# Kernel optimization log

Hardware: AMD Instinct MI355X
Metric: run time of the kernel (lower is better)

Reference implementation:

```python
import jax, jax.numpy as jnp
import numpy as np

HIDDEN = 768
HEADS = 12
HEAD_DIM = HIDDEN // HEADS
INTER = 1152
WINDOW = 128
EPS = 1e-5
ROPE_WAVELENGTH = 10000.0


def setup_inputs() -> dict:
    key = jax.random.key(0)
    ks = jax.random.split(key, 8)
    B, S = 2, 2048
    x = jax.random.normal(ks[0], (B, S, HIDDEN), dtype=jnp.float32)
    padding_mask = jnp.ones((B, S), dtype=jnp.int32)
    sc = 0.02
    wqkv = jax.random.normal(ks[1], (HIDDEN, 3 * HIDDEN), dtype=jnp.float32) * sc
    wo_attn = jax.random.normal(ks[2], (HIDDEN, HIDDEN), dtype=jnp.float32) * sc
    wi0 = jax.random.normal(ks[3], (HIDDEN, INTER), dtype=jnp.float32) * sc
    wi1 = jax.random.normal(ks[4], (HIDDEN, INTER), dtype=jnp.float32) * sc
    wo_mlp = jax.random.normal(ks[5], (INTER, HIDDEN), dtype=jnp.float32) * sc
    g_attn = jnp.ones((HIDDEN,), dtype=jnp.float32)
    g_mlp = jnp.ones((HIDDEN,), dtype=jnp.float32)
    return dict(x=x, padding_mask=padding_mask, wqkv=wqkv, wo_attn=wo_attn,
                wi0=wi0, wi1=wi1, wo_mlp=wo_mlp, g_attn=g_attn, g_mlp=g_mlp)


def _rmsnorm(x, gamma):
    # Keras LayerNormalization(rms_scaling=True): x * rsqrt(mean(x^2)+eps) * gamma
    inv = jax.lax.rsqrt(jnp.mean(jnp.square(x), axis=-1, keepdims=True) + EPS)
    return x * inv * gamma


def _rope(t):
    # t: [B, S, H, D]; standard rotate-half RoPE over the head dim
    S, D = t.shape[1], t.shape[3]
    inv_freq = 1.0 / (ROPE_WAVELENGTH ** (jnp.arange(0, D, 2, dtype=jnp.float32) / D))
    freqs = jnp.arange(S, dtype=jnp.float32)[:, None] * inv_freq[None, :]  # [S, D/2]
    emb = jnp.concatenate([freqs, freqs], axis=-1)  # [S, D]
    cos = jnp.cos(emb)[None, :, None, :]
    sin = jnp.sin(emb)[None, :, None, :]
    h1, h2 = jnp.split(t, 2, axis=-1)
    rot = jnp.concatenate([-h2, h1], axis=-1)
    return t * cos + rot * sin


def reference(x, padding_mask, wqkv, wo_attn, wi0, wi1, wo_mlp, g_attn, g_mlp):
    B, S, _ = x.shape
    # --- attention sub-block ---
    res = x
    h = _rmsnorm(x, g_attn)
    qkv = (h @ wqkv).reshape(B, S, 3, HEADS, HEAD_DIM)
    q, k, v = qkv[:, :, 0], qkv[:, :, 1], qkv[:, :, 2]  # [B, S, H, D]
    q = _rope(q)
    k = _rope(k)
    scores = jnp.einsum('bqhd,bkhd->bhqk', q, k) / jnp.sqrt(
        jnp.asarray(HEAD_DIM, x.dtype))
    pos = jnp.arange(S)
    window = (jnp.abs(pos[:, None] - pos[None, :]) <= WINDOW // 2).astype(jnp.float32)
    mask = window[None, None, :, :] * padding_mask.astype(jnp.float32)[:, None, None, :]
    scores = scores + (1.0 - mask) * -1e9
    attn = jax.nn.softmax(scores, axis=-1)
    out = jnp.einsum('bhqk,bkhd->bqhd', attn, v).reshape(B, S, HIDDEN)
    x = res + out @ wo_attn
    # --- GeGLU MLP sub-block ---
    res = x
    h = _rmsnorm(x, g_mlp)
    h = jax.nn.gelu(h @ wi0, approximate=True) * (h @ wi1)
    return res + h @ wo_mlp
```

## Files before the change

### kernel.cpp

```cpp
#include <hip/hip_runtime.h>
#include <hip/hip_bf16.h>

#define HID 768
#define NHEADS 12
#define HD 64
#define INTER 1152
#define SEQ 2048
#define NB 2
#define ROWS (NB * SEQ)
#define QTA 64
#define KTA 192

typedef __attribute__((ext_vector_type(8))) short bf16x8;
typedef __attribute__((ext_vector_type(4))) float f32x4;

__device__ __forceinline__ float bf2f(unsigned short u) {
    union { unsigned int i; float f; } c; c.i = ((unsigned int)u) << 16; return c.f;
}
__device__ __forceinline__ unsigned short f2bf(float f) {
    union { float f; unsigned int i; } c; c.f = f;
    unsigned int b = c.i;
    b += 0x7FFFu + ((b >> 16) & 1u);
    return (unsigned short)(b >> 16);
}
__device__ __forceinline__ void gload16(const void* g, void* l) {
    __builtin_amdgcn_global_load_lds((const __attribute__((address_space(1))) unsigned int*)g,
                                     (__attribute__((address_space(3))) unsigned int*)l,
                                     16, 0, 0);
}

__global__ __launch_bounds__(256) void rmsnorm_kernel(const float* __restrict__ x,
                                                      const float* __restrict__ g,
                                                      unsigned short* __restrict__ out) {
    int row = blockIdx.x;
    const float* xr = x + (size_t)row * HID;
    unsigned short* orow = out + (size_t)row * HID;
    int tid = threadIdx.x;
    float v0 = xr[tid], v1 = xr[tid + 256], v2 = xr[tid + 512];
    float s = v0 * v0 + v1 * v1 + v2 * v2;
    #pragma unroll
    for (int m = 32; m >= 1; m >>= 1) s += __shfl_xor(s, m, 64);
    __shared__ float red[4];
    if ((tid & 63) == 0) red[tid >> 6] = s;
    __syncthreads();
    float tot = red[0] + red[1] + red[2] + red[3];
    float inv = rsqrtf(tot * (1.0f / HID) + 1e-5f);
    orow[tid]       = f2bf(v0 * inv * g[tid]);
    orow[tid + 256] = f2bf(v1 * inv * g[tid + 256]);
    orow[tid + 512] = f2bf(v2 * inv * g[tid + 512]);
}

__device__ __forceinline__ void wt_tile(const float* __restrict__ W,
                                        unsigned short* __restrict__ Wt,
                                        int K, int N, int bx, int by,
                                        float (*t)[33]) {
    int tx = threadIdx.x & 31, ty = threadIdx.x >> 5;
    #pragma unroll
    for (int i = 0; i < 4; ++i)
        t[ty + i * 8][tx] = W[(size_t)(by * 32 + ty + i * 8) * N + bx * 32 + tx];
    __syncthreads();
    #pragma unroll
    for (int i = 0; i < 4; ++i)
        Wt[(size_t)(bx * 32 + ty + i * 8) * K + by * 32 + tx] = f2bf(t[tx][ty + i * 8]);
}

__global__ __launch_bounds__(256) void prep_kernel(const float* __restrict__ wqkv,
                                                   const float* __restrict__ woa,
                                                   const float* __restrict__ wi0,
                                                   const float* __restrict__ wi1,
                                                   const float* __restrict__ wom,
                                                   unsigned short* __restrict__ wqkvT,
                                                   unsigned short* __restrict__ woaT,
                                                   unsigned short* __restrict__ wi0T,
                                                   unsigned short* __restrict__ wi1T,
                                                   unsigned short* __restrict__ womT,
                                                   float2* __restrict__ rtab) {
    __shared__ float t[32][33];
    int id = blockIdx.x;
    if (id < 1728)       wt_tile(wqkv, wqkvT, 768, 2304, id % 72, id / 72, t);
    else if (id < 2304)  { id -= 1728; wt_tile(woa, woaT, 768, 768, id % 24, id / 24, t); }
    else if (id < 3168)  { id -= 2304; wt_tile(wi0, wi0T, 768, 1152, id % 36, id / 36, t); }
    else if (id < 4032)  { id -= 3168; wt_tile(wi1, wi1T, 768, 1152, id % 36, id / 36, t); }
    else if (id < 4896)  { id -= 4032; wt_tile(wom, womT, 1152, 768, id % 24, id / 24, t); }
    else {
        int idx = (id - 4896) * 256 + threadIdx.x;
        int s = idx >> 5, fi = idx & 31;
        float ang = (float)s * exp2f(-(float)fi * 0.41524101186f);
        float sn, cs;
        sincosf(ang, &sn, &cs);
        rtab[idx] = make_float2(cs, sn);
    }
}

__global__ __launch_bounds__(256) void mfma_gemm64(const unsigned short* __restrict__ A,
                                                   const unsigned short* __restrict__ Bt,
                                                   const float* __restrict__ resid,
                                                   float* __restrict__ C,
                                                   int N, int K, int nbx) {
    __shared__ unsigned short As[64 * 64];
    __shared__ unsigned short Bs[64 * 64];
    int nwg = gridDim.x;
    int bid = blockIdx.x;
    int id2 = (bid & 7) * (nwg >> 3) + (bid >> 3);
    int row0 = (id2 / nbx) * 64, col0 = (id2 % nbx) * 64;
    int tid = threadIdx.x;
    int wave = tid >> 6, lane = tid & 63;
    int wr = wave >> 1, wc = wave & 1;
    int fr = lane & 15, fq = lane >> 4;

    f32x4 acc[2][2];
    #pragma unroll
    for (int m = 0; m < 2; ++m)
        #pragma unroll
        for (int n = 0; n < 2; ++n)
            acc[m][n] = (f32x4){0.f, 0.f, 0.f, 0.f};

    const size_t strideA = (size_t)K * 2;
    const char* Ab = (const char*)A;
    const char* Bb = (const char*)Bt;

    for (int k0 = 0; k0 < K; k0 += 64) {
        #pragma unroll
        for (int r = 0; r < 2; ++r) {
            int L = r * 4096 + tid * 16;
            int row = L >> 7;
            int ss = ((L >> 4) & 7) ^ (row & 7);
            gload16(Ab + (size_t)(row0 + row) * strideA + (size_t)k0 * 2 + ss * 16,
                    (char*)As + L);
            gload16(Bb + (size_t)(col0 + row) * strideA + (size_t)k0 * 2 + ss * 16,
                    (char*)Bs + L);
        }
        __syncthreads();
        bf16x8 af[2][2], bff[2][2];
        #pragma unroll
        for (int m = 0; m < 2; ++m)
            #pragma unroll
            for (int kk = 0; kk < 2; ++kk) {
                int rowa = wr * 32 + m * 16 + fr;
                af[m][kk] = *(const bf16x8*)&As[rowa * 64 + ((kk * 4 + fq) ^ (rowa & 7)) * 8];
                int rowb = wc * 32 + m * 16 + fr;
                bff[m][kk] = *(const bf16x8*)&Bs[rowb * 64 + ((kk * 4 + fq) ^ (rowb & 7)) * 8];
            }
        #pragma unroll
        for (int m = 0; m < 2; ++m)
            #pragma unroll
            for (int n = 0; n < 2; ++n) {
                acc[m][n] = __builtin_amdgcn_mfma_f32_16x16x32_bf16(af[m][0], bff[n][0], acc[m][n], 0, 0, 0);
                acc[m][n] = __builtin_amdgcn_mfma_f32_16x16x32_bf16(af[m][1], bff[n][1], acc[m][n], 0, 0, 0);
            }
        __syncthreads();
    }

    #pragma unroll
    for (int m = 0; m < 2; ++m) {
        #pragma unroll
        for (int j = 0; j < 4; ++j) {
            size_t r = (size_t)(row0 + wr * 32 + m * 16 + fq * 4 + j);
            #pragma unroll
            for (int n = 0; n < 2; ++n) {
                size_t idx = r * N + (col0 + wc * 32 + n * 16 + fr);
                float v = acc[m][n][j];
                if (resid) v += resid[idx];
                C[idx] = v;
            }
        }
    }
}

__global__ __launch_bounds__(256) void gemm_qkv128(const unsigned short* __restrict__ A,
                                                   const unsigned short* __restrict__ Bt,
                                                   const float2* __restrict__ rtab,
                                                   unsigned short* __restrict__ Qb,
                                                   unsigned short* __restrict__ Kb,
                                                   unsigned short* __restrict__ Vt) {
    __shared__ unsigned short As[128 * 64];
    __shared__ unsigned short Bs[64 * 64];
    int bid = blockIdx.x;
    int id2 = (bid & 7) * 144 + (bid >> 3);
    int col0 = (id2 % 36) * 64, row0 = (id2 / 36) * 128;
    int tid = threadIdx.x;
    int wave = tid >> 6, lane = tid & 63;
    int fr = lane & 15, fq = lane >> 4;
    int type = col0 / 768;
    int h = (col0 % 768) >> 6;
    int b = row0 >> 11;
    int s0 = row0 & 2047;
    int bh = b * NHEADS + h;

    f32x4 acc[2][4];
    #pragma unroll
    for (int m = 0; m < 2; ++m)
        #pragma unroll
        for (int n = 0; n < 4; ++n)
            acc[m][n] = (f32x4){0.f, 0.f, 0.f, 0.f};

    const size_t strideA = (size_t)768 * 2;
    const char* Ab = (const char*)A;
    const char* Bb = (const char*)Bt;

    for (int k0 = 0; k0 < 768; k0 += 64) {
        #pragma unroll
        for (int r = 0; r < 4; ++r) {
            int L = r * 4096 + tid * 16;
            int row = L >> 7;
            int ss = ((L >> 4) & 7) ^ (row & 7);
            gload16(Ab + (size_t)(row0 + row) * strideA + (size_t)k0 * 2 + ss * 16,
                    (char*)As + L);
        }
        #pragma unroll
        for (int r = 0; r < 2; ++r) {
            int L = r * 4096 + tid * 16;
            int row = L >> 7;
            int ss = ((L >> 4) & 7) ^ (row & 7);
            gload16(Bb + (size_t)(col0 + row) * strideA + (size_t)k0 * 2 + ss * 16,
                    (char*)Bs + L);
        }
        __syncthreads();
        #pragma unroll
        for (int kk = 0; kk < 2; ++kk) {
            bf16x8 af[2], bf[4];
            #pragma unroll
            for (int m = 0; m < 2; ++m) {
                int rowa = wave * 32 + m * 16 + fr;
                af[m] = *(const bf16x8*)&As[rowa * 64 + ((kk * 4 + fq) ^ (rowa & 7)) * 8];
            }
            #pragma unroll
            for (int n = 0; n < 4; ++n) {
                int rowb = n * 16 + fr;
                bf[n] = *(const bf16x8*)&Bs[rowb * 64 + ((kk * 4 + fq) ^ (rowb & 7)) * 8];
            }
            #pragma unroll
            for (int m = 0; m < 2; ++m)
                #pragma unroll
                for (int n = 0; n < 4; ++n)
                    acc[m][n] = __builtin_amdgcn_mfma_f32_16x16x32_bf16(af[m], bf[n], acc[m][n], 0, 0, 0);
        }
        __syncthreads();
    }

    if (type < 2) {
        unsigned short* P = (type == 0 ? Qb : Kb) + ((size_t)bh * SEQ) * 64;
        #pragma unroll
        for (int m = 0; m < 2; ++m)
            #pragma unroll
            for (int n = 0; n < 4; ++n) {
                int d = n * 16 + fr;
                int fi = d & 31;
                #pragma unroll
                for (int j = 0; j < 4; ++j) {
                    int s = s0 + wave * 32 + m * 16 + fq * 4 + j;
                    float2 cs = rtab[s * 32 + fi];
                    float val = acc[m][n][j], par = acc[m][n ^ 2][j];
                    float o = (d < 32) ? val * cs.x - par * cs.y
                                       : val * cs.x + par * cs.y;
                    P[(size_t)s * 64 + d] = f2bf(o);
                }
            }
    } else {
        unsigned short* vt = As;
        #pragma unroll
        for (int m = 0; m < 2; ++m)
            #pragma unroll
            for (int n = 0; n < 4; ++n) {
                int d = n * 16 + fr;
                #pragma unroll
                for (int j = 0; j < 4; ++j)
                    vt[d * 136 + wave * 32 + m * 16 + fq * 4 + j] = f2bf(acc[m][n][j]);
            }
        __syncthreads();
        int d = tid >> 2, sg = tid & 3;
        unsigned short* vrow = Vt + ((size_t)bh * 64 + d) * SEQ + s0 + sg * 32;
        #pragma unroll
        for (int i = 0; i < 4; ++i)
            *(bf16x8*)(vrow + i * 8) = *(const bf16x8*)&vt[d * 136 + sg * 32 + i * 8];
    }
}

__global__ __launch_bounds__(256) void gemm_ffn128(const unsigned short* __restrict__ A,
                                                   const unsigned short* __restrict__ B0t,
                                                   const unsigned short* __restrict__ B1t,
                                                   unsigned short* __restrict__ O) {
    __shared__ unsigned short As[128 * 64];
    __shared__ unsigned short Bs0[64 * 64];
    __shared__ unsigned short Bs1[64 * 64];
    int bid = blockIdx.x;
    int id2 = (bid & 7) * 72 + (bid >> 3);
    int col0 = (id2 % 18) * 64, row0 = (id2 / 18) * 128;
    int tid = threadIdx.x;
    int wave = tid >> 6, lane = tid & 63;
    int fr = lane & 15, fq = lane >> 4;

    f32x4 acc0[2][4], acc1[2][4];
    #pragma unroll
    for (int m = 0; m < 2; ++m)
        #pragma unroll
        for (int n = 0; n < 4; ++n) {
            acc0[m][n] = (f32x4){0.f, 0.f, 0.f, 0.f};
            acc1[m][n] = (f32x4){0.f, 0.f, 0.f, 0.f};
        }

    const size_t strideA = (size_t)768 * 2;
    const char* Ab  = (const char*)A;
    const char* B0b = (const char*)B0t;
    const char* B1b = (const char*)B1t;

    for (int k0 = 0; k0 < 768; k0 += 64) {
        #pragma unroll
        for (int r = 0; r < 4; ++r) {
            int L = r * 4096 + tid * 16;
            int row = L >> 7;
            int ss = ((L >> 4) & 7) ^ (row & 7);
            gload16(Ab + (size_t)(row0 + row) * strideA + (size_t)k0 * 2 + ss * 16,
                    (char*)As + L);
        }
        #pragma unroll
        for (int r = 0; r < 2; ++r) {
            int L = r * 4096 + tid * 16;
            int row = L >> 7;
            int ss = ((L >> 4) & 7) ^ (row & 7);
            size_t goff = (size_t)(col0 + row) * strideA + (size_t)k0 * 2 + ss * 16;
            gload16(B0b + goff, (char*)Bs0 + L);
            gload16(B1b + goff, (char*)Bs1 + L);
        }
        __syncthreads();
        #pragma unroll
        for (int kk = 0; kk < 2; ++kk) {
            bf16x8 af[2], b0[4], b1[4];
            #pragma unroll
            for (int m = 0; m < 2; ++m) {
                int rowa = wave * 32 + m * 16 + fr;
                af[m] = *(const bf16x8*)&As[rowa * 64 + ((kk * 4 + fq) ^ (rowa & 7)) * 8];
            }
            #pragma unroll
            for (int n = 0; n < 4; ++n) {
                int rowb = n * 16 + fr;
                int sl = ((kk * 4 + fq) ^ (rowb & 7)) * 8;
                b0[n] = *(const bf16x8*)&Bs0[rowb * 64 + sl];
                b1[n] = *(const bf16x8*)&Bs1[rowb * 64 + sl];
            }
            #pragma unroll
            for (int m = 0; m < 2; ++m)
                #pragma unroll
                for (int n = 0; n < 4; ++n) {
                    acc0[m][n] = __builtin_amdgcn_mfma_f32_16x16x32_bf16(af[m], b0[n], acc0[m][n], 0, 0, 0);
                    acc1[m][n] = __builtin_amdgcn_mfma_f32_16x16x32_bf16(af[m], b1[n], acc1[m][n], 0, 0, 0);
                }
        }
        __syncthreads();
    }

    #pragma unroll
    for (int m = 0; m < 2; ++m)
        #pragma unroll
        for (int n = 0; n < 4; ++n)
            #pragma unroll
            for (int j = 0; j < 4; ++j) {
                int r = row0 + wave * 32 + m * 16 + fq * 4 + j;
                float xa = acc0[m][n][j];
                float tn = tanhf(0.7978845608028654f * (xa + 0.044715f * xa * xa * xa));
                float gv = 0.5f * xa * (1.f + tn) * acc1[m][n][j];
                O[(size_t)r * INTER + col0 + n * 16 + fr] = f2bf(gv);
            }
}

__global__ __launch_bounds__(256) void attn_mfma(const unsigned short* __restrict__ Qb,
                                                 const unsigned short* __restrict__ Kb,
                                                 const unsigned short* __restrict__ Vt,
                                                 const int* __restrict__ pmask,
                                                 unsigned short* __restrict__ ao) {
    __shared__ unsigned short Ks[KTA * 64];
    __shared__ unsigned short Vs[64 * KTA];
    __shared__ unsigned short Ps[4][16 * KTA];
    __shared__ float pmsk[KTA];

    int bid = blockIdx.x;
    int qt = bid & 31;
    int h  = (bid >> 5) % NHEADS;
    int b  = bid / (32 * NHEADS);
    int bh = b * NHEADS + h;
    int q0 = qt * QTA;
    int kstart = q0 - 64;
    int tid = threadIdx.x;
    int wave = tid >> 6, lane = tid & 63;
    int fr = lane & 15, fq = lane >> 4;

    const unsigned short* Kg = Kb + ((size_t)bh * SEQ) * 64;
    const unsigned short* Vg = Vt + ((size_t)bh * 64) * SEQ;

    if (tid < KTA) {
        int k = kstart + tid;
        pmsk[tid] = (k >= 0 && k < SEQ) ? (1.0f - (float)pmask[b * SEQ + k]) * -1e9f
                                        : -1e9f;
    }

    bool interior = (qt != 0) && (qt != 31);
    if (interior) {
        #pragma unroll
        for (int r = 0; r < 6; ++r) {
            int c = r * 256 + tid;
            int row = c >> 3, slot = c & 7;
            int ss = slot ^ (row & 7);
            gload16(Kg + (size_t)(kstart + row) * 64 + ss * 8, (char*)Ks + c * 16);
        }
        #pragma unroll
        for (int r = 0; r < 6; ++r) {
            int c = r * 256 + tid;
            int d = c / 24, slot = c - d * 24;
            int ss = (slot & ~7) | ((slot & 7) ^ (d & 7));
            gload16(Vg + (size_t)d * SEQ + kstart + ss * 8, (char*)Vs + c * 16);
        }
    } else {
        #pragma unroll
        for (int r = 0; r < 6; ++r) {
            int c = r * 256 + tid;
            int row = c >> 3, slot = c & 7;
            int ss = slot ^ (row & 7);
            int sk = kstart + row;
            bf16x8 val = {0, 0, 0, 0, 0, 0, 0, 0};
            if (sk >= 0 && sk < SEQ)
                val = *(const bf16x8*)(Kg + (size_t)sk * 64 + ss * 8);
            *(bf16x8*)((char*)Ks + c * 16) = val;
        }
        #pragma unroll
        for (int r = 0; r < 6; ++r) {
            int c = r * 256 + tid;
            int d = c / 24, slot = c - d * 24;
            int ss = (slot & ~7) | ((slot & 7) ^ (d & 7));
            int start = kstart + ss * 8;
            bf16x8 val = {0, 0, 0, 0, 0, 0, 0, 0};
            if (start >= 0 && start + 8 <= SEQ)
                val = *(const bf16x8*)(Vg + (size_t)d * SEQ + start);
            *(bf16x8*)((char*)Vs + c * 16) = val;
        }
    }
    __syncthreads();

    const unsigned short* Qg = Qb + ((size_t)bh * SEQ + q0 + wave * 16 + fr) * 64 + fq * 8;
    bf16x8 qf0 = *(const bf16x8*)(Qg);
    bf16x8 qf1 = *(const bf16x8*)(Qg + 32);

    f32x4 sc[12];
    #pragma unroll
    for (int n = 0; n < 12; ++n) sc[n] = (f32x4){0.f, 0.f, 0.f, 0.f};
    #pragma unroll
    for (int n = 0; n < 12; ++n) {
        int row = n * 16 + fr;
        int base = row * 64;
        bf16x8 k0 = *(const bf16x8*)&Ks[base + ((fq)     ^ (row & 7)) * 8];
        bf16x8 k1 = *(const bf16x8*)&Ks[base + ((4 + fq) ^ (row & 7)) * 8];
        sc[n] = __builtin_amdgcn_mfma_f32_16x16x32_bf16(qf0, k0, sc[n], 0, 0, 0);
        sc[n] = __builtin_amdgcn_mfma_f32_16x16x32_bf16(qf1, k1, sc[n], 0, 0, 0);
    }

    int qrow_base = q0 + wave * 16 + fq * 4;
    float mj[4] = {-1e30f, -1e30f, -1e30f, -1e30f}, sj[4];
    #pragma unroll
    for (int n = 0; n < 12; ++n) {
        int k = kstart + n * 16 + fr;
        float pm = pmsk[n * 16 + fr];
        #pragma unroll
        for (int j = 0; j < 4; ++j) {
            int diff = qrow_base + j - k;
            float s = sc[n][j] * 0.125f + pm;
            if (diff > 64 || diff < -64) s = -1e30f;
            sc[n][j] = s;
            mj[j] = fmaxf(mj[j], s);
        }
    }
    #pragma unroll
    for (int j = 0; j < 4; ++j) {
        #pragma unroll
        for (int mk = 1; mk < 16; mk <<= 1)
            mj[j] = fmaxf(mj[j], __shfl_xor(mj[j], mk, 16));
        sj[j] = 0.f;
    }
    #pragma unroll
    for (int n = 0; n < 12; ++n)
        #pragma unroll
        for (int j = 0; j < 4; ++j) {
            float e = expf(sc[n][j] - mj[j]);
            sc[n][j] = e;
            sj[j] += e;
        }
    #pragma unroll
    for (int j = 0; j < 4; ++j)
        #pragma unroll
        for (int mk = 1; mk < 16; mk <<= 1)
            sj[j] += __shfl_xor(sj[j], mk, 16);

    unsigned short* Pw = Ps[wave];
    #pragma unroll
    for (int n = 0; n < 12; ++n) {
        int slot = n * 2 + (fr >> 3);
        #pragma unroll
        for (int j = 0; j < 4; ++j) {
            int row = fq * 4 + j;
            int ss = (slot & ~7) | ((slot & 7) ^ (row & 7));
            Pw[row * KTA + ss * 8 + (fr & 7)] = f2bf(sc[n][j]);
        }
    }

    f32x4 oacc[4];
    #pragma unroll
    for (int n = 0; n < 4; ++n) oacc[n] = (f32x4){0.f, 0.f, 0.f, 0.f};
    #pragma unroll
    for (int kt = 0; kt < 6; ++kt) {
        int slot = kt * 4 + fq;
        int ssp = (slot & ~7) | ((slot & 7) ^ (fr & 7));
        bf16x8 pa = *(const bf16x8*)&Pw[fr * KTA + ssp * 8];
        #pragma unroll
        for (int n = 0; n < 4; ++n) {
            int d = n * 16 + fr;
            int ssv = (slot & ~7) | ((slot & 7) ^ (d & 7));
            bf16x8 vf = *(const bf16x8*)&Vs[d * KTA + ssv * 8];
            oacc[n] = __builtin_amdgcn_mfma_f32_16x16x32_bf16(pa, vf, oacc[n], 0, 0, 0);
        }
    }

    unsigned short* aob = ao + ((size_t)(b * SEQ + qrow_base)) * HID + h * 64;
    float rs[4];
    #pragma unroll
    for (int j = 0; j < 4; ++j) rs[j] = 1.0f / sj[j];
    #pragma unroll
    for (int n = 0; n < 4; ++n)
        #pragma unroll
        for (int j = 0; j < 4; ++j)
            aob[(size_t)j * HID + n * 16 + fr] = f2bf(oacc[n][j] * rs[j]);
}

extern "C" void kernel_launch(void* const* d_in, const int* in_sizes, int n_in,
                              void* d_out, int out_size, void* d_ws, size_t ws_size,
                              hipStream_t stream) {
    const float* x       = (const float*)d_in[0];
    const int*   pmask   = (const int*)d_in[1];
    const float* wqkv    = (const float*)d_in[2];
    const float* wo_attn = (const float*)d_in[3];
    const float* wi0     = (const float*)d_in[4];
    const float* wi1     = (const float*)d_in[5];
    const float* wo_mlp  = (const float*)d_in[6];
    const float* g_attn  = (const float*)d_in[7];
    const float* g_mlp   = (const float*)d_in[8];
    float* out = (float*)d_out;

    char* w = (char*)d_ws;
    unsigned short* hbf   = (unsigned short*)(w);
    unsigned short* aobf  = (unsigned short*)(w + 6291456);
    unsigned short* Qb    = (unsigned short*)(w + 12582912);
    unsigned short* Kb    = (unsigned short*)(w + 18874368);
    unsigned short* Vt    = (unsigned short*)(w + 25165824);
    unsigned short* mgate = (unsigned short*)(w + 31457280);
    float2*         rtab  = (float2*)(w + 40894464);
    unsigned short* wqkvT = (unsigned short*)(w + 41418752);
    unsigned short* woaT  = (unsigned short*)(w + 44957696);
    unsigned short* wi0T  = (unsigned short*)(w + 46137344);
    unsigned short* wi1T  = (unsigned short*)(w + 47906816);
    unsigned short* womT  = (unsigned short*)(w + 49676288);

    prep_kernel<<<5152, 256, 0, stream>>>(wqkv, wo_attn, wi0, wi1, wo_mlp,
                                          wqkvT, woaT, wi0T, wi1T, womT, rtab);
    rmsnorm_kernel<<<ROWS, 256, 0, stream>>>(x, g_attn, hbf);
    gemm_qkv128<<<1152, 256, 0, stream>>>(hbf, wqkvT, rtab, Qb, Kb, Vt);
    attn_mfma<<<NB * NHEADS * (SEQ / QTA), 256, 0, stream>>>(Qb, Kb, Vt, pmask, aobf);
    mfma_gemm64<<<768, 256, 0, stream>>>(aobf, woaT, x, out, 768, 768, 12);
    rmsnorm_kernel<<<ROWS, 256, 0, stream>>>(out, g_mlp, hbf);
    gemm_ffn128<<<576, 256, 0, stream>>>(hbf, wi0T, wi1T, mgate);
    mfma_gemm64<<<768, 256, 0, stream>>>(mgate, womT, out, out, 768, 1152, 12);
}
```

Baseline: 128.3 us.

## Merge weight prep with first RMSNorm, widen GEMM K-tiles, hoist Q loads

Folds the first RMSNorm into the weight-transpose/RoPE-table prep kernel so one launch does both. mfma_gemm64 and gemm_qkv128 now stage 128-wide K tiles in LDS with a 16-way XOR swizzle, which halves the barrier and loop count. The price is double the LDS per block, which can reduce occupancy. The attention kernel now issues the Q fragment loads before K/V staging so their latency overlaps.

```diff
diff --git a/kernel.cpp b/kernel.cpp
--- a/kernel.cpp
+++ b/kernel.cpp
@@ -29,6 +29,70 @@
                                      16, 0, 0);
 }
 
+__device__ __forceinline__ void wt_tile(const float* __restrict__ W,
+                                        unsigned short* __restrict__ Wt,
+                                        int K, int N, int bx, int by,
+                                        float (*t)[33]) {
+    int tx = threadIdx.x & 31, ty = threadIdx.x >> 5;
+    #pragma unroll
+    for (int i = 0; i < 4; ++i)
+        t[ty + i * 8][tx] = W[(size_t)(by * 32 + ty + i * 8) * N + bx * 32 + tx];
+    __syncthreads();
+    #pragma unroll
+    for (int i = 0; i < 4; ++i)
+        Wt[(size_t)(bx * 32 + ty + i * 8) * K + by * 32 + tx] = f2bf(t[tx][ty + i * 8]);
+}
+
+__global__ __launch_bounds__(256) void prep_rms_kernel(const float* __restrict__ x,
+                                                       const float* __restrict__ g,
+                                                       unsigned short* __restrict__ hbf,
+                                                       const float* __restrict__ wqkv,
+                                                       const float* __restrict__ woa,
+                                                       const float* __restrict__ wi0,
+                                                       const float* __restrict__ wi1,
+                                                       const float* __restrict__ wom,
+                                                       unsigned short* __restrict__ wqkvT,
+                                                       unsigned short* __restrict__ woaT,
+                                                       unsigned short* __restrict__ wi0T,
+                                                       unsigned short* __restrict__ wi1T,
+                                                       unsigned short* __restrict__ womT,
+                                                       float2* __restrict__ rtab) {
+    __shared__ float t[32][33];
+    __shared__ float red[4];
+    int id = blockIdx.x;
+    int tid = threadIdx.x;
+    if (id < 4096) {
+        const float* xr = x + (size_t)id * HID;
+        unsigned short* orow = hbf + (size_t)id * HID;
+        float v0 = xr[tid], v1 = xr[tid + 256], v2 = xr[tid + 512];
+        float s = v0 * v0 + v1 * v1 + v2 * v2;
+        #pragma unroll
+        for (int m = 32; m >= 1; m >>= 1) s += __shfl_xor(s, m, 64);
+        if ((tid & 63) == 0) red[tid >> 6] = s;
+        __syncthreads();
+        float tot = red[0] + red[1] + red[2] + red[3];
+        float inv = rsqrtf(tot * (1.0f / HID) + 1e-5f);
+        orow[tid]       = f2bf(v0 * inv * g[tid]);
+        orow[tid + 256] = f2bf(v1 * inv * g[tid + 256]);
+        orow[tid + 512] = f2bf(v2 * inv * g[tid + 512]);
+        return;
+    }
+    id -= 4096;
+    if (id < 1728)       wt_tile(wqkv, wqkvT, 768, 2304, id % 72, id / 72, t);
+    else if (id < 2304)  { id -= 1728; wt_tile(woa, woaT, 768, 768, id % 24, id / 24, t); }
+    else if (id < 3168)  { id -= 2304; wt_tile(wi0, wi0T, 768, 1152, id % 36, id / 36, t); }
+    else if (id < 4032)  { id -= 3168; wt_tile(wi1, wi1T, 768, 1152, id % 36, id / 36, t); }
+    else if (id < 4896)  { id -= 4032; wt_tile(wom, womT, 1152, 768, id % 24, id / 24, t); }
+    else {
+        int idx = (id - 4896) * 256 + tid;
+        int s = idx >> 5, fi = idx & 31;
+        float ang = (float)s * exp2f(-(float)fi * 0.41524101186f);
+        float sn, cs;
+        sincosf(ang, &sn, &cs);
+        rtab[idx] = make_float2(cs, sn);
+    }
+}
+
 __global__ __launch_bounds__(256) void rmsnorm_kernel(const float* __restrict__ x,
                                                       const float* __restrict__ g,
                                                       unsigned short* __restrict__ out) {
@@ -50,55 +114,13 @@
     orow[tid + 512] = f2bf(v2 * inv * g[tid + 512]);
 }
 
-__device__ __forceinline__ void wt_tile(const float* __restrict__ W,
-                                        unsigned short* __restrict__ Wt,
-                                        int K, int N, int bx, int by,
-                                        float (*t)[33]) {
-    int tx = threadIdx.x & 31, ty = threadIdx.x >> 5;
-    #pragma unroll
-    for (int i = 0; i < 4; ++i)
-        t[ty + i * 8][tx] = W[(size_t)(by * 32 + ty + i * 8) * N + bx * 32 + tx];
-    __syncthreads();
-    #pragma unroll
-    for (int i = 0; i < 4; ++i)
-        Wt[(size_t)(bx * 32 + ty + i * 8) * K + by * 32 + tx] = f2bf(t[tx][ty + i * 8]);
-}
-
-__global__ __launch_bounds__(256) void prep_kernel(const float* __restrict__ wqkv,
-                                                   const float* __restrict__ woa,
-                                                   const float* __restrict__ wi0,
-                                                   const float* __restrict__ wi1,
-                                                   const float* __restrict__ wom,
-                                                   unsigned short* __restrict__ wqkvT,
-                                                   unsigned short* __restrict__ woaT,
-                                                   unsigned short* __restrict__ wi0T,
-                                                   unsigned short* __restrict__ wi1T,
-                                                   unsigned short* __restrict__ womT,
-                                                   float2* __restrict__ rtab) {
-    __shared__ float t[32][33];
-    int id = blockIdx.x;
-    if (id < 1728)       wt_tile(wqkv, wqkvT, 768, 2304, id % 72, id / 72, t);
-    else if (id < 2304)  { id -= 1728; wt_tile(woa, woaT, 768, 768, id % 24, id / 24, t); }
-    else if (id < 3168)  { id -= 2304; wt_tile(wi0, wi0T, 768, 1152, id % 36, id / 36, t); }
-    else if (id < 4032)  { id -= 3168; wt_tile(wi1, wi1T, 768, 1152, id % 36, id / 36, t); }
-    else if (id < 4896)  { id -= 4032; wt_tile(wom, womT, 1152, 768, id % 24, id / 24, t); }
-    else {
-        int idx = (id - 4896) * 256 + threadIdx.x;
-        int s = idx >> 5, fi = idx & 31;
-        float ang = (float)s * exp2f(-(float)fi * 0.41524101186f);
-        float sn, cs;
-        sincosf(ang, &sn, &cs);
-        rtab[idx] = make_float2(cs, sn);
-    }
-}
-
 __global__ __launch_bounds__(256) void mfma_gemm64(const unsigned short* __restrict__ A,
                                                    const unsigned short* __restrict__ Bt,
                                                    const float* __restrict__ resid,
                                                    float* __restrict__ C,
                                                    int N, int K, int nbx) {
-    __shared__ unsigned short As[64 * 64];
-    __shared__ unsigned short Bs[64 * 64];
+    __shared__ unsigned short As[64 * 128];
+    __shared__ unsigned short Bs[64 * 128];
     int nwg = gridDim.x;
     int bid = blockIdx.x;
     int id2 = (bid & 7) * (nwg >> 3) + (bid >> 3);
@@ -108,46 +130,47 @@
     int wr = wave >> 1, wc = wave & 1;
     int fr = lane & 15, fq = lane >> 4;
 
-    f32x4 acc[2][2];
-    #pragma unroll
-    for (int m = 0; m < 2; ++m)
-        #pragma unroll
-        for (int n = 0; n < 2; ++n)
-            acc[m][n] = (f32x4){0.f, 0.f, 0.f, 0.f};
-
     const size_t strideA = (size_t)K * 2;
     const char* Ab = (const char*)A;
     const char* Bb = (const char*)Bt;
 
-    for (int k0 = 0; k0 < K; k0 += 64) {
-        #pragma unroll
-        for (int r = 0; r < 2; ++r) {
+    f32x4 acc[2][2];
+    #pragma unroll
+    for (int m = 0; m < 2; ++m)
+        #pragma unroll
+        for (int n = 0; n < 2; ++n)
+            acc[m][n] = (f32x4){0.f, 0.f, 0.f, 0.f};
+
+    int nt = K >> 7;
+    for (int t = 0; t < nt; ++t) {
+        int k0 = t << 7;
+        #pragma unroll
+        for (int r = 0; r < 4; ++r) {
             int L = r * 4096 + tid * 16;
-            int row = L >> 7;
-            int ss = ((L >> 4) & 7) ^ (row & 7);
+            int row = L >> 8;
+            int ss = ((L >> 4) & 15) ^ (row & 15);
             gload16(Ab + (size_t)(row0 + row) * strideA + (size_t)k0 * 2 + ss * 16,
                     (char*)As + L);
             gload16(Bb + (size_t)(col0 + row) * strideA + (size_t)k0 * 2 + ss * 16,
                     (char*)Bs + L);
         }
         __syncthreads();
-        bf16x8 af[2][2], bff[2][2];
-        #pragma unroll
-        for (int m = 0; m < 2; ++m)
-            #pragma unroll
-            for (int kk = 0; kk < 2; ++kk) {
+        #pragma unroll
+        for (int kk = 0; kk < 4; ++kk) {
+            bf16x8 af[2], bff[2];
+            #pragma unroll
+            for (int m = 0; m < 2; ++m) {
                 int rowa = wr * 32 + m * 16 + fr;
-                af[m][kk] = *(const bf16x8*)&As[rowa * 64 + ((kk * 4 + fq) ^ (rowa & 7)) * 8];
+                af[m] = *(const bf16x8*)&As[rowa * 128 + (((kk * 4 + fq)) ^ (rowa & 15)) * 8];
                 int rowb = wc * 32 + m * 16 + fr;
-                bff[m][kk] = *(const bf16x8*)&Bs[rowb * 64 + ((kk * 4 + fq) ^ (rowb & 7)) * 8];
-            }
-        #pragma unroll
-        for (int m = 0; m < 2; ++m)
-            #pragma unroll
-            for (int n = 0; n < 2; ++n) {
-                acc[m][n] = __builtin_amdgcn_mfma_f32_16x16x32_bf16(af[m][0], bff[n][0], acc[m][n], 0, 0, 0);
-                acc[m][n] = __builtin_amdgcn_mfma_f32_16x16x32_bf16(af[m][1], bff[n][1], acc[m][n], 0, 0, 0);
-            }
+                bff[m] = *(const bf16x8*)&Bs[rowb * 128 + (((kk * 4 + fq)) ^ (rowb & 15)) * 8];
+            }
+            #pragma unroll
+            for (int m = 0; m < 2; ++m)
+                #pragma unroll
+                for (int n = 0; n < 2; ++n)
+                    acc[m][n] = __builtin_amdgcn_mfma_f32_16x16x32_bf16(af[m], bff[n], acc[m][n], 0, 0, 0);
+        }
         __syncthreads();
     }
 
@@ -173,8 +196,8 @@
                                                    unsigned short* __restrict__ Qb,
                                                    unsigned short* __restrict__ Kb,
                                                    unsigned short* __restrict__ Vt) {
-    __shared__ unsigned short As[128 * 64];
-    __shared__ unsigned short Bs[64 * 64];
+    __shared__ unsigned short As[128 * 128];
+    __shared__ unsigned short Bs[64 * 128];
     int bid = blockIdx.x;
     int id2 = (bid & 7) * 144 + (bid >> 3);
     int col0 = (id2 % 36) * 64, row0 = (id2 / 36) * 128;
@@ -187,47 +210,48 @@
     int s0 = row0 & 2047;
     int bh = b * NHEADS + h;
 
-    f32x4 acc[2][4];
-    #pragma unroll
-    for (int m = 0; m < 2; ++m)
-        #pragma unroll
-        for (int n = 0; n < 4; ++n)
-            acc[m][n] = (f32x4){0.f, 0.f, 0.f, 0.f};
-
     const size_t strideA = (size_t)768 * 2;
     const char* Ab = (const char*)A;
     const char* Bb = (const char*)Bt;
 
-    for (int k0 = 0; k0 < 768; k0 += 64) {
+    f32x4 acc[2][4];
+    #pragma unroll
+    for (int m = 0; m < 2; ++m)
+        #pragma unroll
+        for (int n = 0; n < 4; ++n)
+            acc[m][n] = (f32x4){0.f, 0.f, 0.f, 0.f};
+
+    for (int t = 0; t < 6; ++t) {
+        int k0 = t << 7;
+        #pragma unroll
+        for (int r = 0; r < 8; ++r) {
+            int L = r * 4096 + tid * 16;
+            int row = L >> 8;
+            int ss = ((L >> 4) & 15) ^ (row & 15);
+            gload16(Ab + (size_t)(row0 + row) * strideA + (size_t)k0 * 2 + ss * 16,
+                    (char*)As + L);
+        }
         #pragma unroll
         for (int r = 0; r < 4; ++r) {
             int L = r * 4096 + tid * 16;
-            int row = L >> 7;
-            int ss = ((L >> 4) & 7) ^ (row & 7);
-            gload16(Ab + (size_t)(row0 + row) * strideA + (size_t)k0 * 2 + ss * 16,
-                    (char*)As + L);
-        }
-        #pragma unroll
-        for (int r = 0; r < 2; ++r) {
-            int L = r * 4096 + tid * 16;
-            int row = L >> 7;
-            int ss = ((L >> 4) & 7) ^ (row & 7);
+            int row = L >> 8;
+            int ss = ((L >> 4) & 15) ^ (row & 15);
             gload16(Bb + (size_t)(col0 + row) * strideA + (size_t)k0 * 2 + ss * 16,
                     (char*)Bs + L);
         }
         __syncthreads();
         #pragma unroll
-        for (int kk = 0; kk < 2; ++kk) {
+        for (int kk = 0; kk < 4; ++kk) {
             bf16x8 af[2], bf[4];
             #pragma unroll
             for (int m = 0; m < 2; ++m) {
                 int rowa = wave * 32 + m * 16 + fr;
-                af[m] = *(const bf16x8*)&As[rowa * 64 + ((kk * 4 + fq) ^ (rowa & 7)) * 8];
+                af[m] = *(const bf16x8*)&As[rowa * 128 + ((kk * 4 + fq) ^ (rowa & 15)) * 8];
             }
             #pragma unroll
             for (int n = 0; n < 4; ++n) {
                 int rowb = n * 16 + fr;
-                bf[n] = *(const bf16x8*)&Bs[rowb * 64 + ((kk * 4 + fq) ^ (rowb & 7)) * 8];
+                bf[n] = *(const bf16x8*)&Bs[rowb * 128 + ((kk * 4 + fq) ^ (rowb & 15)) * 8];
             }
             #pragma unroll
             for (int m = 0; m < 2; ++m)
@@ -387,6 +411,9 @@
     const unsigned short* Kg = Kb + ((size_t)bh * SEQ) * 64;
     const unsigned short* Vg = Vt + ((size_t)bh * 64) * SEQ;
 
+    const unsigned short* Qg = Qb + ((size_t)bh * SEQ + q0 + wave * 16 + fr) * 64 + fq * 8;
+    bf16x8 qf0 = *(const bf16x8*)(Qg);
+    bf16x8 qf1 = *(const bf16x8*)(Qg + 32);
     if (tid < KTA) {
         int k = kstart + tid;
         pmsk[tid] = (k >= 0 && k < SEQ) ? (1.0f - (float)pmask[b * SEQ + k]) * -1e9f
@@ -434,10 +461,6 @@
         }
     }
     __syncthreads();
-
-    const unsigned short* Qg = Qb + ((size_t)bh * SEQ + q0 + wave * 16 + fr) * 64 + fq * 8;
-    bf16x8 qf0 = *(const bf16x8*)(Qg);
-    bf16x8 qf1 = *(const bf16x8*)(Qg + 32);
 
     f32x4 sc[12];
     #pragma unroll
@@ -556,9 +579,9 @@
     unsigned short* wi1T  = (unsigned short*)(w + 47906816);
     unsigned short* womT  = (unsigned short*)(w + 49676288);
 
-    prep_kernel<<<5152, 256, 0, stream>>>(wqkv, wo_attn, wi0, wi1, wo_mlp,
-                                          wqkvT, woaT, wi0T, wi1T, womT, rtab);
-    rmsnorm_kernel<<<ROWS, 256, 0, stream>>>(x, g_attn, hbf);
+    prep_rms_kernel<<<4096 + 5152, 256, 0, stream>>>(x, g_attn, hbf,
+                                                     wqkv, wo_attn, wi0, wi1, wo_mlp,
+                                                     wqkvT, woaT, wi0T, wi1T, womT, rtab);
     gemm_qkv128<<<1152, 256, 0, stream>>>(hbf, wqkvT, rtab, Qb, Kb, Vt);
     attn_mfma<<<NB * NHEADS * (SEQ / QTA), 256, 0, stream>>>(Qb, Kb, Vt, pmask, aobf);
     mfma_gemm64<<<768, 256, 0, stream>>>(aobf, woaT, x, out, 768, 768, 12);
```

Measured after the change: 122.5 us. -4.5%, faster.
